# Performance work log

Hardware: AMD Instinct MI355X
Metric: run time of the kernel (lower is better)

## Reference

```python
import jax, jax.numpy as jnp
import numpy as np

LUT_DIM = 33  # standard 33^3 color LUT


def setup_inputs() -> dict:
    key = jax.random.key(0)
    k1, k2 = jax.random.split(key)
    # learned 3D LUT: [out_channels=3, D_b, D_g, D_r]
    lut = jax.random.normal(k1, (3, LUT_DIM, LUT_DIM, LUT_DIM), dtype=jnp.float32) * 0.1
    # input image batch in [0, 1): [B, 3, H, W]
    x = jax.random.uniform(k2, (4, 3, 1024, 1024), dtype=jnp.float32)
    return {"lut": lut, "x": x}


def reference(lut, x):
    """Trilinear interpolation of a 3D color LUT (image-adaptive-3DLUT forward).

    lut: [3, D, D, D] laid out as lut[c, ib, ig, ir] (flat index ir + ig*D + ib*D*D)
    x:   [B, 3, H, W] with channels (r, g, b) in [0, 1]
    returns: [B, 3, H, W]
    """
    dim = lut.shape[-1]
    scale = dim - 1  # 1 / binsize

    r, g, b = x[:, 0], x[:, 1], x[:, 2]  # each [B, H, W]

    def cell(c):
        s = c * scale
        idx = jnp.clip(jnp.floor(s), 0, scale - 1).astype(jnp.int32)
        return idx, s - idx.astype(s.dtype)  # integer cell, fractional offset

    ir, dr = cell(r)
    ig, dg = cell(g)
    ib, db = cell(b)

    lut_flat = lut.reshape(3, -1)  # [3, D^3], tiny and cache-resident

    out = jnp.zeros((3,) + r.shape, dtype=x.dtype)  # [3, B, H, W]
    # 8 corners of the enclosing LUT cell, trilinear weights
    for or_ in (0, 1):
        wr = dr if or_ else (1.0 - dr)
        for og in (0, 1):
            wg = dg if og else (1.0 - dg)
            for ob in (0, 1):
                wb = db if ob else (1.0 - db)
                flat = ((ib + ob) * dim + (ig + og)) * dim + (ir + or_)  # [B, H, W]
                corner = lut_flat[:, flat]  # gather -> [3, B, H, W]
                out = out + (wr * wg * wb)[None] * corner

    return jnp.transpose(out, (1, 0, 2, 3))  # [B, 3, H, W]
```

## Files before the change

kernel.cpp:

```cpp
#include <hip/hip_runtime.h>
#include <hip/hip_fp16.h>


#define LUT_D   33
#define LUT_DD  (LUT_D * LUT_D)
#define LUT_N   (LUT_D * LUT_D * LUT_D)
#define HW4     (1024 * 1024 / 4)
#define NGROUPS (4 * HW4)
#define NCHUNKS 256
#define THREADS 1024
#define ITERS   (NGROUPS / NCHUNKS / THREADS)
#define STAGE4  (35936 / 4)

__device__ __forceinline__ unsigned int pack2(float a, float b) {
    __half2 h = __floats2half2_rn(a, b);
    return *(unsigned int*)&h;
}

__device__ __forceinline__ float2 unpack2(unsigned int p) {
    __half2 h = *(__half2*)&p;
    return __half22float2(h);
}

__global__ __launch_bounds__(THREADS)
void lut3d_trilerp_kernel(const float* __restrict__ lut,
                          const float* __restrict__ x,
                          float* __restrict__ out) {
    extern __shared__ __align__(16) unsigned int P[];

    const int bx    = blockIdx.x;
    const int c     = bx % 3;
    const int chunk = bx / 3;

    const float* lc = lut + c * LUT_N;

    for (int i4 = threadIdx.x; i4 < STAGE4; i4 += THREADS) {
        const int i = i4 * 4;
        const float4 v  = *(const float4*)(lc + i);
        const float  v4 = lc[i + 4];
        uint4 w;
        w.x = pack2(v.x, v.y);
        w.y = pack2(v.y, v.z);
        w.z = pack2(v.z, v.w);
        w.w = pack2(v.w, v4);
        *(uint4*)(P + i) = w;
    }
    if (threadIdx.x == 0) {
        P[LUT_N - 1] = pack2(lc[LUT_N - 1], 0.0f);
    }
    __syncthreads();

    const float4* x4 = (const float4*)x;
    float4*       o4 = (float4*)out;

    const int g0 = chunk * (NGROUPS / NCHUNKS) + (int)threadIdx.x;

#pragma unroll
    for (int it = 0; it < ITERS; ++it) {
        const int g     = g0 + it * THREADS;
        const int b_img = g >> 18;
        const int hw4   = g & (HW4 - 1);
        const int ibase = b_img * 3 * HW4 + hw4;

        const float4 r4 = x4[ibase];
        const float4 g4 = x4[ibase + HW4];
        const float4 b4 = x4[ibase + 2 * HW4];

        const float rr[4] = {r4.x, r4.y, r4.z, r4.w};
        const float gg[4] = {g4.x, g4.y, g4.z, g4.w};
        const float bb[4] = {b4.x, b4.y, b4.z, b4.w};
        float oo[4];

#pragma unroll
        for (int k = 0; k < 4; ++k) {
            const float sr = rr[k] * 32.0f;
            const float sg = gg[k] * 32.0f;
            const float sb = bb[k] * 32.0f;
            float fr = fminf(fmaxf(floorf(sr), 0.0f), 31.0f);
            float fg = fminf(fmaxf(floorf(sg), 0.0f), 31.0f);
            float fb = fminf(fmaxf(floorf(sb), 0.0f), 31.0f);
            const float dr = sr - fr;
            const float dg = sg - fg;
            const float db = sb - fb;
            const int ir = (int)fr, ig = (int)fg, ib = (int)fb;
            const int idx = (ib * LUT_D + ig) * LUT_D + ir;

            const float2 a00 = unpack2(P[idx]);
            const float2 a01 = unpack2(P[idx + LUT_D]);
            const float2 a10 = unpack2(P[idx + LUT_DD]);
            const float2 a11 = unpack2(P[idx + LUT_DD + LUT_D]);

            const float l00 = a00.x + dr * (a00.y - a00.x);
            const float l01 = a01.x + dr * (a01.y - a01.x);
            const float l10 = a10.x + dr * (a10.y - a10.x);
            const float l11 = a11.x + dr * (a11.y - a11.x);
            const float l0  = l00 + dg * (l01 - l00);
            const float l1  = l10 + dg * (l11 - l10);
            oo[k] = l0 + db * (l1 - l0);
        }

        o4[(b_img * 3 + c) * HW4 + hw4] = make_float4(oo[0], oo[1], oo[2], oo[3]);
    }
}

extern "C" void kernel_launch(void* const* d_in, const int* in_sizes, int n_in,
                              void* d_out, int out_size, void* d_ws, size_t ws_size,
                              hipStream_t stream) {
    const float* lut = (const float*)d_in[0];
    const float* x   = (const float*)d_in[1];
    float*       out = (float*)d_out;

    const int grid = 3 * NCHUNKS;
    const size_t lds_bytes = LUT_N * sizeof(unsigned int);

    lut3d_trilerp_kernel<<<grid, THREADS, lds_bytes, stream>>>(lut, x, out);
}
```

Measured before the change: 122.9 us.

## Prepack LUT once and stage via direct global-to-LDS loads, prefetch inputs

Adds a small pre-pass kernel that packs each LUT entry with its r-neighbor into half2 words in workspace, so each main-kernel block copies the packed table into LDS with global_load_lds DMA instead of converting it per block. Block-to-channel/chunk mapping is reordered to group work by XCD. All input float4s for a thread are loaded up front, LDS reads are batched before the math, and outputs use nontemporal stores. The cost is an extra kernel launch and higher register pressure from holding every iteration's inputs at once.

Measured after the change: 118.0 us. 1.04x faster.

```diff
diff --git a/kernel.cpp b/kernel.cpp
--- a/kernel.cpp
+++ b/kernel.cpp
@@ -2,51 +2,61 @@
 #include <hip/hip_fp16.h>
 
 
-#define LUT_D   33
-#define LUT_DD  (LUT_D * LUT_D)
-#define LUT_N   (LUT_D * LUT_D * LUT_D)
-#define HW4     (1024 * 1024 / 4)
-#define NGROUPS (4 * HW4)
-#define NCHUNKS 256
-#define THREADS 1024
-#define ITERS   (NGROUPS / NCHUNKS / THREADS)
-#define STAGE4  (35936 / 4)
+#define LUT_D     33
+#define LUT_DD    (LUT_D * LUT_D)
+#define LUT_N     (LUT_D * LUT_D * LUT_D)
+#define CH_STRIDE 35940
+#define STAGE_G   (CH_STRIDE / 4)
+#define HW4       (1024 * 1024 / 4)
+#define NGROUPS   (4 * HW4)
+#define NCHUNKS   256
+#define THREADS   1024
+#define ITERS     (NGROUPS / NCHUNKS / THREADS)
+
+typedef float vfloat4 __attribute__((ext_vector_type(4)));
 
 __device__ __forceinline__ unsigned int pack2(float a, float b) {
-    __half2 h = __floats2half2_rn(a, b);
-    return *(unsigned int*)&h;
+    union { __half2 h; unsigned int u; } cv;
+    cv.h = __floats2half2_rn(a, b);
+    return cv.u;
+}
+__device__ __forceinline__ float2 unpack2(unsigned int p) {
+    union { unsigned int u; __half2 h; } cv;
+    cv.u = p;
+    return __half22float2(cv.h);
 }
 
-__device__ __forceinline__ float2 unpack2(unsigned int p) {
-    __half2 h = *(__half2*)&p;
-    return __half22float2(h);
+__global__ __launch_bounds__(256)
+void lut_pack_kernel(const float* __restrict__ lut, unsigned int* __restrict__ W) {
+    const int t = blockIdx.x * 256 + (int)threadIdx.x;
+    if (t >= 3 * LUT_N) return;
+    const int c = t / LUT_N;
+    const int i = t - c * LUT_N;
+    const float a = lut[t];
+    const float b = (i + 1 < LUT_N) ? lut[t + 1] : 0.0f;
+    W[c * CH_STRIDE + i] = pack2(a, b);
 }
 
 __global__ __launch_bounds__(THREADS)
-void lut3d_trilerp_kernel(const float* __restrict__ lut,
+void lut3d_trilerp_kernel(const unsigned int* __restrict__ W,
                           const float* __restrict__ x,
                           float* __restrict__ out) {
     extern __shared__ __align__(16) unsigned int P[];
 
-    const int bx    = blockIdx.x;
-    const int c     = bx % 3;
-    const int chunk = bx / 3;
+    const int bx   = blockIdx.x;
+    const int xcd  = bx & 7;
+    const int c    = (bx >> 3) % 3;
+    const int chunk = (bx / 24) * 8 + xcd;
 
-    const float* lc = lut + c * LUT_N;
-
-    for (int i4 = threadIdx.x; i4 < STAGE4; i4 += THREADS) {
-        const int i = i4 * 4;
-        const float4 v  = *(const float4*)(lc + i);
-        const float  v4 = lc[i + 4];
-        uint4 w;
-        w.x = pack2(v.x, v.y);
-        w.y = pack2(v.y, v.z);
-        w.z = pack2(v.z, v.w);
-        w.w = pack2(v.w, v4);
-        *(uint4*)(P + i) = w;
-    }
-    if (threadIdx.x == 0) {
-        P[LUT_N - 1] = pack2(lc[LUT_N - 1], 0.0f);
+    const unsigned int* src = W + c * CH_STRIDE;
+    for (int s = 0; s < 9; ++s) {
+        const int gid = s * THREADS + (int)threadIdx.x;
+        if (gid < STAGE_G) {
+            __builtin_amdgcn_global_load_lds(
+                (const __attribute__((address_space(1))) void*)(src + gid * 4),
+                (__attribute__((address_space(3))) void*)(P + gid * 4),
+                16, 0, 0);
+        }
     }
     __syncthreads();
 
@@ -55,63 +65,84 @@
 
     const int g0 = chunk * (NGROUPS / NCHUNKS) + (int)threadIdx.x;
 
+    float4 R[ITERS], G[ITERS], B[ITERS];
+    int obase[ITERS];
 #pragma unroll
     for (int it = 0; it < ITERS; ++it) {
         const int g     = g0 + it * THREADS;
         const int b_img = g >> 18;
         const int hw4   = g & (HW4 - 1);
         const int ibase = b_img * 3 * HW4 + hw4;
+        R[it] = x4[ibase];
+        G[it] = x4[ibase + HW4];
+        B[it] = x4[ibase + 2 * HW4];
+        obase[it] = ibase + c * HW4;
+    }
 
-        const float4 r4 = x4[ibase];
-        const float4 g4 = x4[ibase + HW4];
-        const float4 b4 = x4[ibase + 2 * HW4];
+#pragma unroll
+    for (int it = 0; it < ITERS; ++it) {
+        const float rr[4] = {R[it].x, R[it].y, R[it].z, R[it].w};
+        const float gg[4] = {G[it].x, G[it].y, G[it].z, G[it].w};
+        const float bb[4] = {B[it].x, B[it].y, B[it].z, B[it].w};
 
-        const float rr[4] = {r4.x, r4.y, r4.z, r4.w};
-        const float gg[4] = {g4.x, g4.y, g4.z, g4.w};
-        const float bb[4] = {b4.x, b4.y, b4.z, b4.w};
-        float oo[4];
-
+        int   idx[4];
+        float dr[4], dg[4], db[4];
 #pragma unroll
         for (int k = 0; k < 4; ++k) {
             const float sr = rr[k] * 32.0f;
             const float sg = gg[k] * 32.0f;
             const float sb = bb[k] * 32.0f;
-            float fr = fminf(fmaxf(floorf(sr), 0.0f), 31.0f);
-            float fg = fminf(fmaxf(floorf(sg), 0.0f), 31.0f);
-            float fb = fminf(fmaxf(floorf(sb), 0.0f), 31.0f);
-            const float dr = sr - fr;
-            const float dg = sg - fg;
-            const float db = sb - fb;
-            const int ir = (int)fr, ig = (int)fg, ib = (int)fb;
-            const int idx = (ib * LUT_D + ig) * LUT_D + ir;
-
-            const float2 a00 = unpack2(P[idx]);
-            const float2 a01 = unpack2(P[idx + LUT_D]);
-            const float2 a10 = unpack2(P[idx + LUT_DD]);
-            const float2 a11 = unpack2(P[idx + LUT_DD + LUT_D]);
-
-            const float l00 = a00.x + dr * (a00.y - a00.x);
-            const float l01 = a01.x + dr * (a01.y - a01.x);
-            const float l10 = a10.x + dr * (a10.y - a10.x);
-            const float l11 = a11.x + dr * (a11.y - a11.x);
-            const float l0  = l00 + dg * (l01 - l00);
-            const float l1  = l10 + dg * (l11 - l10);
-            oo[k] = l0 + db * (l1 - l0);
+            const float fr = fminf(fmaxf(floorf(sr), 0.0f), 31.0f);
+            const float fg = fminf(fmaxf(floorf(sg), 0.0f), 31.0f);
+            const float fb = fminf(fmaxf(floorf(sb), 0.0f), 31.0f);
+            dr[k] = sr - fr;
+            dg[k] = sg - fg;
+            db[k] = sb - fb;
+            idx[k] = ((int)fb * LUT_D + (int)fg) * LUT_D + (int)fr;
         }
 
-        o4[(b_img * 3 + c) * HW4 + hw4] = make_float4(oo[0], oo[1], oo[2], oo[3]);
+        unsigned int q00[4], q01[4], q10[4], q11[4];
+#pragma unroll
+        for (int k = 0; k < 4; ++k) {
+            q00[k] = P[idx[k]];
+            q01[k] = P[idx[k] + LUT_D];
+            q10[k] = P[idx[k] + LUT_DD];
+            q11[k] = P[idx[k] + LUT_DD + LUT_D];
+        }
+
+        float oo[4];
+#pragma unroll
+        for (int k = 0; k < 4; ++k) {
+            const float2 a00 = unpack2(q00[k]);
+            const float2 a01 = unpack2(q01[k]);
+            const float2 a10 = unpack2(q10[k]);
+            const float2 a11 = unpack2(q11[k]);
+            const float l00 = a00.x + dr[k] * (a00.y - a00.x);
+            const float l01 = a01.x + dr[k] * (a01.y - a01.x);
+            const float l10 = a10.x + dr[k] * (a10.y - a10.x);
+            const float l11 = a11.x + dr[k] * (a11.y - a11.x);
+            const float l0  = l00 + dg[k] * (l01 - l00);
+            const float l1  = l10 + dg[k] * (l11 - l10);
+            oo[k] = l0 + db[k] * (l1 - l0);
+        }
+
+        vfloat4 v = {oo[0], oo[1], oo[2], oo[3]};
+        __builtin_nontemporal_store(v, (vfloat4*)&o4[obase[it]]);
     }
 }
 
 extern "C" void kernel_launch(void* const* d_in, const int* in_sizes, int n_in,
                               void* d_out, int out_size, void* d_ws, size_t ws_size,
                               hipStream_t stream) {
-    const float* lut = (const float*)d_in[0];
-    const float* x   = (const float*)d_in[1];
-    float*       out = (float*)d_out;
+    const float*  lut = (const float*)d_in[0];
+    const float*  x   = (const float*)d_in[1];
+    float*        out = (float*)d_out;
+    unsigned int* W   = (unsigned int*)d_ws;
+
+    const int pack_grid = (3 * LUT_N + 255) / 256;
+    lut_pack_kernel<<<pack_grid, 256, 0, stream>>>(lut, W);
 
     const int grid = 3 * NCHUNKS;
-    const size_t lds_bytes = LUT_N * sizeof(unsigned int);
-
-    lut3d_trilerp_kernel<<<grid, THREADS, lds_bytes, stream>>>(lut, x, out);
+    const size_t lds_bytes = (size_t)STAGE_G * 16;
+    lut3d_trilerp_kernel<<<grid, THREADS, lds_bytes, stream>>>(W, x, out);
 }
```
